# Kernel tuning notes

Hardware: AMD Instinct MI355X
Metric: run time of the kernel (lower is better)

The kernel has to match this reference:

```python
import jax, jax.numpy as jnp
import numpy as np

WINDOW_SIZE = 35

def setup_inputs() -> dict:
    key = jax.random.key(0)
    k1, k2 = jax.random.split(key)
    B, T, U = 4096, WINDOW_SIZE, 1024
    x = jax.random.normal(k1, (B, T, U), dtype=jnp.float32)
    # nn.Linear(units*2, units): weight [units, units*2], bias [units]
    W = jax.random.normal(k2, (U, 2 * U), dtype=jnp.float32) * (1.0 / np.sqrt(2 * U))
    b = jnp.zeros((U,), dtype=jnp.float32)
    return {"x": x, "W": W, "b": b}

def reference(x, W, b):
    # x: [B, T, U]; hidden init zeros [B, U]
    B, T, U = x.shape
    # split weight into input part and hidden part (concat order: [x_t, h])
    Wx = W[:, :U]   # [U, U]
    Wh = W[:, U:]   # [U, U]

    def step(h, x_t):
        # out = relu([x_t, h] @ W^T + b)
        h_new = jax.nn.relu(x_t @ Wx.T + h @ Wh.T + b)
        return h_new, None

    h0 = jnp.zeros((B, U), dtype=x.dtype)
    x_time_major = jnp.swapaxes(x, 0, 1)  # [T, B, U]
    h_final, _ = jax.lax.scan(step, h0, x_time_major)
    return h_final
```

## Files before the change

### kernel.cpp

```cpp
#include <hip/hip_runtime.h>


typedef __bf16 bf16;
typedef __bf16 bf16x8 __attribute__((ext_vector_type(8)));
typedef __bf16 bf16x4 __attribute__((ext_vector_type(4)));
typedef float f32x4 __attribute__((ext_vector_type(4)));

#define B_N 4096
#define T_N 35
#define U_N 1024
#define K_N 2048
#define XROW (T_N * U_N)

#define AS1CP(p) ((const __attribute__((address_space(1))) void*)(p))
#define AS3CP(p) ((__attribute__((address_space(3))) void*)(p))

__global__ __launch_bounds__(256) void w_to_bf16(const float* __restrict__ W,
                                                 bf16* __restrict__ Wb) {
  int i = (blockIdx.x * 256 + threadIdx.x) * 4;
  f32x4 f = *(const f32x4*)(W + i);
  bf16x4 o = { (bf16)f.x, (bf16)f.y, (bf16)f.z, (bf16)f.w };
  *(bf16x4*)(Wb + i) = o;
}

__global__ __launch_bounds__(256) void rnn_step(
    const float* __restrict__ x,
    int t,
    const bf16* __restrict__ Wb,
    const bf16* __restrict__ hin,
    const float* __restrict__ bias,
    bf16* __restrict__ hout,
    float* __restrict__ out)
{
  __shared__ bf16 As[128 * 32];
  __shared__ bf16 Bs[128 * 32];

  const int tid  = threadIdx.x;
  const int w    = tid >> 6;
  const int l    = tid & 63;
  const int row0 = blockIdx.x * 128;
  const int col0 = blockIdx.y * 128;
  const int wm   = w & 1;
  const int wn   = w >> 1;

  const int lq = l >> 4;
  const int lm = l & 15;
  const int lk = lq * 8;

  const int arow = w * 32;
  const int srow = l >> 2;
  const int scol = (l & 3) * 8;

  f32x4 acc[4][4] = {};

  for (int kk = 0; kk < 1024; kk += 32) {
#pragma unroll
    for (int r = 0; r < 2; ++r) {
      int nr = arow + r * 16;
      const bf16* g = Wb + (size_t)(col0 + nr + srow) * K_N + kk + scol;
      __builtin_amdgcn_global_load_lds(AS1CP(g), AS3CP(Bs + nr * 32), 16, 0, 0);
    }
#pragma unroll
    for (int r = 0; r < 2; ++r) {
      int c   = tid + r * 256;
      int row = c >> 2;
      int cc  = (c & 3) * 8;
      const float* g = x + (size_t)(row0 + row) * XROW + (size_t)t * U_N + kk + cc;
      f32x4 f0 = *(const f32x4*)g;
      f32x4 f1 = *(const f32x4*)(g + 4);
      bf16x8 v = { (bf16)f0.x, (bf16)f0.y, (bf16)f0.z, (bf16)f0.w,
                   (bf16)f1.x, (bf16)f1.y, (bf16)f1.z, (bf16)f1.w };
      *(bf16x8*)(As + row * 32 + cc) = v;
    }
    __syncthreads();

    bf16x8 af[4], bfr[4];
#pragma unroll
    for (int mi = 0; mi < 4; ++mi)
      af[mi] = *(const bf16x8*)(As + (wm * 64 + mi * 16 + lm) * 32 + lk);
#pragma unroll
    for (int ni = 0; ni < 4; ++ni)
      bfr[ni] = *(const bf16x8*)(Bs + (wn * 64 + ni * 16 + lm) * 32 + lk);
#pragma unroll
    for (int mi = 0; mi < 4; ++mi)
#pragma unroll
      for (int ni = 0; ni < 4; ++ni)
        acc[mi][ni] = __builtin_amdgcn_mfma_f32_16x16x32_bf16(af[mi], bfr[ni],
                                                              acc[mi][ni], 0, 0, 0);
    __syncthreads();
  }

  for (int kk = 1024; kk < 2048; kk += 32) {
#pragma unroll
    for (int r = 0; r < 2; ++r) {
      int nr = arow + r * 16;
      const bf16* g = Wb + (size_t)(col0 + nr + srow) * K_N + kk + scol;
      __builtin_amdgcn_global_load_lds(AS1CP(g), AS3CP(Bs + nr * 32), 16, 0, 0);
    }
#pragma unroll
    for (int r = 0; r < 2; ++r) {
      int nr = arow + r * 16;
      const bf16* g = hin + (size_t)(row0 + nr + srow) * U_N + (kk - 1024) + scol;
      __builtin_amdgcn_global_load_lds(AS1CP(g), AS3CP(As + nr * 32), 16, 0, 0);
    }
    __syncthreads();

    bf16x8 af[4], bfr[4];
#pragma unroll
    for (int mi = 0; mi < 4; ++mi)
      af[mi] = *(const bf16x8*)(As + (wm * 64 + mi * 16 + lm) * 32 + lk);
#pragma unroll
    for (int ni = 0; ni < 4; ++ni)
      bfr[ni] = *(const bf16x8*)(Bs + (wn * 64 + ni * 16 + lm) * 32 + lk);
#pragma unroll
    for (int mi = 0; mi < 4; ++mi)
#pragma unroll
      for (int ni = 0; ni < 4; ++ni)
        acc[mi][ni] = __builtin_amdgcn_mfma_f32_16x16x32_bf16(af[mi], bfr[ni],
                                                              acc[mi][ni], 0, 0, 0);
    __syncthreads();
  }

#pragma unroll
  for (int ni = 0; ni < 4; ++ni) {
    int col = col0 + wn * 64 + ni * 16 + lm;
    float bv = bias[col];
#pragma unroll
    for (int mi = 0; mi < 4; ++mi) {
#pragma unroll
      for (int i = 0; i < 4; ++i) {
        int row = row0 + wm * 64 + mi * 16 + lq * 4 + i;
        float v = acc[mi][ni][i] + bv;
        v = v > 0.f ? v : 0.f;
        hout[(size_t)row * U_N + col] = (bf16)v;
        if (out) out[(size_t)row * U_N + col] = v;
      }
    }
  }
}

extern "C" void kernel_launch(void* const* d_in, const int* in_sizes, int n_in,
                              void* d_out, int out_size, void* d_ws, size_t ws_size,
                              hipStream_t stream) {
  const float* x    = (const float*)d_in[0];
  const float* W    = (const float*)d_in[1];
  const float* bias = (const float*)d_in[2];
  float* out = (float*)d_out;

  char* ws = (char*)d_ws;
  bf16* Wb = (bf16*)ws;
  bf16* h0 = (bf16*)(ws + (size_t)4 * 1024 * 1024);
  bf16* h1 = (bf16*)(ws + (size_t)12 * 1024 * 1024);

  w_to_bf16<<<2048, 256, 0, stream>>>(W, Wb);
  hipMemsetAsync(h0, 0, (size_t)B_N * U_N * sizeof(bf16), stream);

  bf16* bufs[2] = { h0, h1 };
  dim3 grid(32, 8);
  for (int t = 0; t < T_N; ++t) {
    bf16* hin  = bufs[t & 1];
    bf16* hout = bufs[(t + 1) & 1];
    float* o   = (t == T_N - 1) ? out : nullptr;
    rnn_step<<<grid, dim3(256), 0, stream>>>(x, t, Wb, hin, bias, hout, o);
  }
}
```

Measured before the change: 2.692 ms.

## Hoist input projection into one batched GEMM, leaving recurrent-only step kernels

```diff
diff --git a/kernel.cpp b/kernel.cpp
--- a/kernel.cpp
+++ b/kernel.cpp
@@ -9,115 +9,86 @@
 #define B_N 4096
 #define T_N 35
 #define U_N 1024
-#define K_N 2048
 #define XROW (T_N * U_N)
+#define BU (B_N * U_N)
 
 #define AS1CP(p) ((const __attribute__((address_space(1))) void*)(p))
 #define AS3CP(p) ((__attribute__((address_space(3))) void*)(p))
 
-__global__ __launch_bounds__(256) void w_to_bf16(const float* __restrict__ W,
-                                                 bf16* __restrict__ Wb) {
+__global__ __launch_bounds__(256) void pack_w(const float* __restrict__ W,
+                                              bf16* __restrict__ Wxb,
+                                              bf16* __restrict__ Whb) {
   int i = (blockIdx.x * 256 + threadIdx.x) * 4;
-  f32x4 f = *(const f32x4*)(W + i);
-  bf16x4 o = { (bf16)f.x, (bf16)f.y, (bf16)f.z, (bf16)f.w };
-  *(bf16x4*)(Wb + i) = o;
-}
-
-__global__ __launch_bounds__(256) void rnn_step(
-    const float* __restrict__ x,
-    int t,
-    const bf16* __restrict__ Wb,
-    const bf16* __restrict__ hin,
-    const float* __restrict__ bias,
-    bf16* __restrict__ hout,
-    float* __restrict__ out)
+  int n = i >> 10, k = i & 1023;
+  f32x4 a = *(const f32x4*)(W + (size_t)n * 2048 + k);
+  f32x4 b = *(const f32x4*)(W + (size_t)n * 2048 + 1024 + k);
+  bf16x4 av = { (bf16)a.x, (bf16)a.y, (bf16)a.z, (bf16)a.w };
+  bf16x4 bv = { (bf16)b.x, (bf16)b.y, (bf16)b.z, (bf16)b.w };
+  *(bf16x4*)(Wxb + i) = av;
+  *(bf16x4*)(Whb + i) = bv;
+}
+
+__global__ __launch_bounds__(256) void z_gemm(
+    const float* __restrict__ x, const bf16* __restrict__ Wxb,
+    const float* __restrict__ bias, bf16* __restrict__ Zb)
 {
-  __shared__ bf16 As[128 * 32];
-  __shared__ bf16 Bs[128 * 32];
-
-  const int tid  = threadIdx.x;
-  const int w    = tid >> 6;
-  const int l    = tid & 63;
-  const int row0 = blockIdx.x * 128;
-  const int col0 = blockIdx.y * 128;
-  const int wm   = w & 1;
-  const int wn   = w >> 1;
-
-  const int lq = l >> 4;
-  const int lm = l & 15;
-  const int lk = lq * 8;
-
-  const int arow = w * 32;
-  const int srow = l >> 2;
-  const int scol = (l & 3) * 8;
+  __shared__ bf16 As[128 * 64];
+  __shared__ bf16 Bs[128 * 64];
+
+  const int tid = threadIdx.x;
+  const int w = tid >> 6, l = tid & 63;
+  const int mt = blockIdx.y;
+  const int t = mt >> 5;
+  const int row0 = (mt & 31) << 7;
+  const int col0 = blockIdx.x << 7;
+  const int wm = w & 1, wn = w >> 1;
+  const int lq = l >> 4, lm = l & 15;
+  const int lrow8 = l >> 3, lc = l & 7;
+  const int clog = lc ^ lrow8;
 
   f32x4 acc[4][4] = {};
-
-  for (int kk = 0; kk < 1024; kk += 32) {
-#pragma unroll
-    for (int r = 0; r < 2; ++r) {
-      int nr = arow + r * 16;
-      const bf16* g = Wb + (size_t)(col0 + nr + srow) * K_N + kk + scol;
-      __builtin_amdgcn_global_load_lds(AS1CP(g), AS3CP(Bs + nr * 32), 16, 0, 0);
-    }
-#pragma unroll
-    for (int r = 0; r < 2; ++r) {
-      int c   = tid + r * 256;
-      int row = c >> 2;
-      int cc  = (c & 3) * 8;
-      const float* g = x + (size_t)(row0 + row) * XROW + (size_t)t * U_N + kk + cc;
+  const float* xbase = x + (size_t)row0 * XROW + (size_t)t * U_N;
+
+  for (int kk = 0; kk < 1024; kk += 64) {
+#pragma unroll
+    for (int r = 0; r < 4; ++r) {
+      int nr = w * 32 + r * 8;
+      const bf16* g = Wxb + (size_t)(col0 + nr + lrow8) * U_N + kk + clog * 8;
+      __builtin_amdgcn_global_load_lds(AS1CP(g), AS3CP(Bs + nr * 64), 16, 0, 0);
+    }
+#pragma unroll
+    for (int i = 0; i < 4; ++i) {
+      int row = i * 32 + (tid >> 3);
+      int c = tid & 7;
+      const float* g = xbase + (size_t)row * XROW + kk + c * 8;
       f32x4 f0 = *(const f32x4*)g;
       f32x4 f1 = *(const f32x4*)(g + 4);
       bf16x8 v = { (bf16)f0.x, (bf16)f0.y, (bf16)f0.z, (bf16)f0.w,
                    (bf16)f1.x, (bf16)f1.y, (bf16)f1.z, (bf16)f1.w };
-      *(bf16x8*)(As + row * 32 + cc) = v;
-    }
-    __syncthreads();
-
-    bf16x8 af[4], bfr[4];
-#pragma unroll
-    for (int mi = 0; mi < 4; ++mi)
-      af[mi] = *(const bf16x8*)(As + (wm * 64 + mi * 16 + lm) * 32 + lk);
-#pragma unroll
-    for (int ni = 0; ni < 4; ++ni)
-      bfr[ni] = *(const bf16x8*)(Bs + (wn * 64 + ni * 16 + lm) * 32 + lk);
-#pragma unroll
-    for (int mi = 0; mi < 4; ++mi)
-#pragma unroll
-      for (int ni = 0; ni < 4; ++ni)
-        acc[mi][ni] = __builtin_amdgcn_mfma_f32_16x16x32_bf16(af[mi], bfr[ni],
-                                                              acc[mi][ni], 0, 0, 0);
-    __syncthreads();
-  }
-
-  for (int kk = 1024; kk < 2048; kk += 32) {
-#pragma unroll
-    for (int r = 0; r < 2; ++r) {
-      int nr = arow + r * 16;
-      const bf16* g = Wb + (size_t)(col0 + nr + srow) * K_N + kk + scol;
-      __builtin_amdgcn_global_load_lds(AS1CP(g), AS3CP(Bs + nr * 32), 16, 0, 0);
-    }
-#pragma unroll
-    for (int r = 0; r < 2; ++r) {
-      int nr = arow + r * 16;
-      const bf16* g = hin + (size_t)(row0 + nr + srow) * U_N + (kk - 1024) + scol;
-      __builtin_amdgcn_global_load_lds(AS1CP(g), AS3CP(As + nr * 32), 16, 0, 0);
-    }
-    __syncthreads();
-
-    bf16x8 af[4], bfr[4];
-#pragma unroll
-    for (int mi = 0; mi < 4; ++mi)
-      af[mi] = *(const bf16x8*)(As + (wm * 64 + mi * 16 + lm) * 32 + lk);
-#pragma unroll
-    for (int ni = 0; ni < 4; ++ni)
-      bfr[ni] = *(const bf16x8*)(Bs + (wn * 64 + ni * 16 + lm) * 32 + lk);
-#pragma unroll
-    for (int mi = 0; mi < 4; ++mi)
-#pragma unroll
-      for (int ni = 0; ni < 4; ++ni)
-        acc[mi][ni] = __builtin_amdgcn_mfma_f32_16x16x32_bf16(af[mi], bfr[ni],
-                                                              acc[mi][ni], 0, 0, 0);
+      *(bf16x8*)(As + row * 64 + ((c ^ (row & 7)) << 3)) = v;
+    }
+    __syncthreads();
+
+#pragma unroll
+    for (int kq = 0; kq < 2; ++kq) {
+      bf16x8 af[4], bfr[4];
+#pragma unroll
+      for (int mi = 0; mi < 4; ++mi) {
+        int r = wm * 64 + mi * 16 + lm;
+        af[mi] = *(const bf16x8*)(As + r * 64 + (((kq * 4 + lq) ^ (r & 7)) << 3));
+      }
+#pragma unroll
+      for (int ni = 0; ni < 4; ++ni) {
+        int r = wn * 64 + ni * 16 + lm;
+        bfr[ni] = *(const bf16x8*)(Bs + r * 64 + (((kq * 4 + lq) ^ (r & 7)) << 3));
+      }
+#pragma unroll
+      for (int mi = 0; mi < 4; ++mi)
+#pragma unroll
+        for (int ni = 0; ni < 4; ++ni)
+          acc[mi][ni] = __builtin_amdgcn_mfma_f32_16x16x32_bf16(af[mi], bfr[ni],
+                                                                acc[mi][ni], 0, 0, 0);
+    }
     __syncthreads();
   }
 
@@ -127,10 +98,81 @@
     float bv = bias[col];
 #pragma unroll
     for (int mi = 0; mi < 4; ++mi) {
+      int rbase = row0 + wm * 64 + mi * 16 + lq * 4;
+#pragma unroll
+      for (int i = 0; i < 4; ++i)
+        Zb[(size_t)t * BU + (size_t)(rbase + i) * U_N + col] = (bf16)(acc[mi][ni][i] + bv);
+    }
+  }
+}
+
+__global__ __launch_bounds__(256) void rnn_step(
+    const bf16* __restrict__ hin, const bf16* __restrict__ Whb,
+    const bf16* __restrict__ Zt, bf16* __restrict__ hout,
+    float* __restrict__ out)
+{
+  __shared__ bf16 As[128 * 64];
+  __shared__ bf16 Bs[64 * 64];
+
+  const int tid = threadIdx.x;
+  const int w = tid >> 6, l = tid & 63;
+  const int col0 = blockIdx.x << 6;
+  const int row0 = blockIdx.y << 7;
+  const int wm = w & 1, wn = w >> 1;
+  const int lq = l >> 4, lm = l & 15;
+  const int lrow8 = l >> 3, lc = l & 7;
+  const int clog = lc ^ lrow8;
+
+  f32x4 acc[4][2] = {};
+
+  for (int kk = 0; kk < 1024; kk += 64) {
+#pragma unroll
+    for (int r = 0; r < 4; ++r) {
+      int nr = w * 32 + r * 8;
+      const bf16* g = hin + (size_t)(row0 + nr + lrow8) * U_N + kk + clog * 8;
+      __builtin_amdgcn_global_load_lds(AS1CP(g), AS3CP(As + nr * 64), 16, 0, 0);
+    }
+#pragma unroll
+    for (int r = 0; r < 2; ++r) {
+      int nr = w * 16 + r * 8;
+      const bf16* g = Whb + (size_t)(col0 + nr + lrow8) * U_N + kk + clog * 8;
+      __builtin_amdgcn_global_load_lds(AS1CP(g), AS3CP(Bs + nr * 64), 16, 0, 0);
+    }
+    __syncthreads();
+
+#pragma unroll
+    for (int kq = 0; kq < 2; ++kq) {
+      bf16x8 af[4], bfr[2];
+#pragma unroll
+      for (int mi = 0; mi < 4; ++mi) {
+        int r = wm * 64 + mi * 16 + lm;
+        af[mi] = *(const bf16x8*)(As + r * 64 + (((kq * 4 + lq) ^ (r & 7)) << 3));
+      }
+#pragma unroll
+      for (int ni = 0; ni < 2; ++ni) {
+        int r = wn * 32 + ni * 16 + lm;
+        bfr[ni] = *(const bf16x8*)(Bs + r * 64 + (((kq * 4 + lq) ^ (r & 7)) << 3));
+      }
+#pragma unroll
+      for (int mi = 0; mi < 4; ++mi)
+#pragma unroll
+        for (int ni = 0; ni < 2; ++ni)
+          acc[mi][ni] = __builtin_amdgcn_mfma_f32_16x16x32_bf16(af[mi], bfr[ni],
+                                                                acc[mi][ni], 0, 0, 0);
+    }
+    __syncthreads();
+  }
+
+#pragma unroll
+  for (int ni = 0; ni < 2; ++ni) {
+    int col = col0 + wn * 32 + ni * 16 + lm;
+#pragma unroll
+    for (int mi = 0; mi < 4; ++mi) {
+      int rbase = row0 + wm * 64 + mi * 16 + lq * 4;
 #pragma unroll
       for (int i = 0; i < 4; ++i) {
-        int row = row0 + wm * 64 + mi * 16 + lq * 4 + i;
-        float v = acc[mi][ni][i] + bv;
+        int row = rbase + i;
+        float v = acc[mi][ni][i] + (float)Zt[(size_t)row * U_N + col];
         v = v > 0.f ? v : 0.f;
         hout[(size_t)row * U_N + col] = (bf16)v;
         if (out) out[(size_t)row * U_N + col] = v;
@@ -148,19 +190,22 @@
   float* out = (float*)d_out;
 
   char* ws = (char*)d_ws;
-  bf16* Wb = (bf16*)ws;
-  bf16* h0 = (bf16*)(ws + (size_t)4 * 1024 * 1024);
-  bf16* h1 = (bf16*)(ws + (size_t)12 * 1024 * 1024);
-
-  w_to_bf16<<<2048, 256, 0, stream>>>(W, Wb);
-  hipMemsetAsync(h0, 0, (size_t)B_N * U_N * sizeof(bf16), stream);
+  bf16* Wxb = (bf16*)ws;
+  bf16* Whb = (bf16*)(ws + ((size_t)2 << 20));
+  bf16* h0  = (bf16*)(ws + ((size_t)4 << 20));
+  bf16* h1  = (bf16*)(ws + ((size_t)12 << 20));
+  bf16* Zb  = (bf16*)(ws + ((size_t)32 << 20));
+
+  pack_w<<<1024, 256, 0, stream>>>(W, Wxb, Whb);
+  hipMemsetAsync(h0, 0, (size_t)BU * sizeof(bf16), stream);
+
+  z_gemm<<<dim3(8, 1120), 256, 0, stream>>>(x, Wxb, bias, Zb);
 
   bf16* bufs[2] = { h0, h1 };
-  dim3 grid(32, 8);
   for (int t = 0; t < T_N; ++t) {
     bf16* hin  = bufs[t & 1];
     bf16* hout = bufs[(t + 1) & 1];
     float* o   = (t == T_N - 1) ? out : nullptr;
-    rnn_step<<<grid, dim3(256), 0, stream>>>(x, t, Wb, hin, bias, hout, o);
-  }
-}
+    rnn_step<<<dim3(16, 32), 256, 0, stream>>>(hin, Whb, Zb + (size_t)t * BU, hout, o);
+  }
+}
```

After: 2.239 ms. 16.8% less time.
